# Optimization experiments

Hardware: AMD Instinct MI355X
Metric: run time of the kernel (lower is better)

The kernel has to match this reference:

```python
import jax, jax.numpy as jnp
import numpy as np

T, D_IN, H, D_OUT = 20, 4, 768, 1
B = 1024


def setup_inputs() -> dict:
    key = jax.random.key(0)
    ks = jax.random.split(key, 8)
    s = 1.0 / np.sqrt(H)
    return {
        "batch_price": jax.random.normal(ks[0], (B, T, D_IN), jnp.float32),
        "batch_event": jax.random.normal(ks[1], (B, T, H), jnp.float32),
        "W_ih": jax.random.uniform(ks[2], (T, 4 * H, D_IN), jnp.float32, -s, s),
        "W_hh": jax.random.uniform(ks[3], (T, 4 * H, H), jnp.float32, -s, s),
        "b_ih": jax.random.uniform(ks[4], (T, 4 * H), jnp.float32, -s, s),
        "b_hh": jax.random.uniform(ks[5], (T, 4 * H), jnp.float32, -s, s),
        "fc_w": jax.random.uniform(ks[6], (D_OUT, H), jnp.float32, -s, s),
        "fc_b": jax.random.uniform(ks[7], (D_OUT,), jnp.float32, -s, s),
    }


def _lstm_cell(x, h_mat, c, wih, whh, bih, bhh):
    # gates: [B, 4H] in PyTorch LSTMCell order (i, f, g, o)
    gates = x @ wih.T + bih + h_mat @ whh.T + bhh
    i, f, g, o = jnp.split(gates, 4, axis=-1)
    c_next = jax.nn.sigmoid(f) * c + jax.nn.sigmoid(i) * jnp.tanh(g)
    h_next = jax.nn.sigmoid(o) * jnp.tanh(c_next)
    return h_next, c_next


def reference(batch_price, batch_event, W_ih, W_hh, b_ih, b_hh, fc_w, fc_b):
    Bb, Tt, _ = batch_price.shape
    Hh = W_hh.shape[-1]
    # step 0: hx = batch_event[:, 0], cell state = zeros
    h, c = _lstm_cell(batch_price[:, 0], batch_event[:, 0],
                      jnp.zeros((Bb, Hh), batch_price.dtype),
                      W_ih[0], W_hh[0], b_ih[0], b_hh[0])

    def step(carry, inp):
        h, c = carry
        x, ev, wih, whh, bih, bhh = inp
        # faithful to source: hx = torch.sum(batch_event_t + h_prev) -> scalar
        hx = jnp.sum(ev + h)
        h_mat = jnp.broadcast_to(hx, (Bb, Hh))
        h2, c2 = _lstm_cell(x, h_mat, c, wih, whh, bih, bhh)
        return (h2, c2), None

    xs = (jnp.swapaxes(batch_price[:, 1:], 0, 1),  # [T-1, B, D_IN]
          jnp.swapaxes(batch_event[:, 1:], 0, 1),  # [T-1, B, H]
          W_ih[1:], W_hh[1:], b_ih[1:], b_hh[1:])
    (h, c), _ = jax.lax.scan(step, (h, c), xs)
    return h @ fc_w.T + fc_b  # [B, 1]
```

## Files before the change

kernel.cpp:

```cpp
#include <hip/hip_runtime.h>
#include <stdint.h>

#define Bsz 1024
#define Tn  20
#define Hn  768
#define G4n 3072

#define WS_SH    0
#define WS_SEV   32
#define WS_PART  64
#define WS_BCAST 576
#define WS_RS    640
#define WS_BS    62080
#define WS_C     123520
#define WS_EVH   909952
#define WS_EVL   1303168
#define WS_WH    1696384
#define WS_WL    2581120

#define NBC_EV   512
#define NBC_W    1152
#define NBC_Z    3
#define NBC_TOT  (NBC_EV + NBC_W + NBC_Z)

#define NB_GEMM   768
#define NB_ROWSUM 1824
#define NB_SEV    608
#define NB_BIAS   60
#define NB_TOTAL  (NB_GEMM + NB_ROWSUM + NB_SEV + NB_BIAS)

typedef float  floatx4 __attribute__((ext_vector_type(4)));
typedef short  bfrag8  __attribute__((ext_vector_type(8)));

__device__ __forceinline__ float wave_reduce(float v){
#pragma unroll
    for (int o = 32; o > 0; o >>= 1) v += __shfl_down(v, o, 64);
    return v;
}
__device__ __forceinline__ float sigf(float x){ return 1.0f/(1.0f+__expf(-x)); }
__device__ __forceinline__ float tanhfast(float x){ return 2.0f/(1.0f+__expf(-2.0f*x)) - 1.0f; }
__device__ __forceinline__ unsigned short f2bf(float f){
    uint32_t u = __float_as_uint(f);
    return (unsigned short)((u + 0x7fffu + ((u>>16)&1u)) >> 16);
}
__device__ __forceinline__ float bf2f(unsigned short h){ return __uint_as_float(((uint32_t)h)<<16); }
__device__ __forceinline__ uint64_t pack_tv(unsigned t, float v){
    return ((uint64_t)t << 32) | (uint64_t)__float_as_uint(v);
}

__global__ __launch_bounds__(256) void k_conv(
    const float* __restrict__ ev, const float* __restrict__ whh,
    float* __restrict__ ws)
{
    int bid = blockIdx.x, tid = threadIdx.x;
    if (bid < NBC_EV + NBC_W) {
        if (tid >= 192) return;
        int r = tid / 96;
        int i = (tid - r*96) * 8;
        const float* src;
        unsigned short *dh, *dl;
        int prow;
        if (bid < NBC_EV) {
            prow = bid*2 + r;
            src = ev + (size_t)prow*(Tn*Hn) + i;
            dh = (unsigned short*)(ws + WS_EVH);
            dl = (unsigned short*)(ws + WS_EVL);
        } else {
            int p = (bid - NBC_EV)*2 + r;
            int gsel = p / Hn;
            int ga = (gsel==0) ? 0 : (gsel==1 ? 2 : 3);
            int j = ga*Hn + (p - gsel*Hn);
            prow = p;
            src = whh + (size_t)j*Hn + i;
            dh = (unsigned short*)(ws + WS_WH);
            dl = (unsigned short*)(ws + WS_WL);
        }
        int rb = prow >> 4, col = prow & 15;
        int kb = i >> 5, q = (i >> 3) & 3;
        size_t base = (((size_t)(rb*24 + kb))*64 + q*16 + col) * 8;

        float4 v0 = *(const float4*)src;
        float4 v1 = *(const float4*)(src+4);
        float f[8] = {v0.x,v0.y,v0.z,v0.w,v1.x,v1.y,v1.z,v1.w};
        bfrag8 hv, lv;
#pragma unroll
        for (int qq = 0; qq < 8; ++qq) {
            unsigned short hb = f2bf(f[qq]);
            hv[qq] = (short)hb;
            lv[qq] = (short)f2bf(f[qq] - bf2f(hb));
        }
        *(bfrag8*)(dh + base) = hv;
        *(bfrag8*)(dl + base) = lv;
    } else {
        int idx = (bid - NBC_EV - NBC_W)*256 + tid;
        if (idx < 640) ws[idx] = 0.0f;
    }
}

__global__ __launch_bounds__(256) void k_pre(
    const float* __restrict__ price, const float* __restrict__ ev,
    const float* __restrict__ wih,   const float* __restrict__ whh,
    const float* __restrict__ bih,   const float* __restrict__ bhh,
    float* __restrict__ ws)
{
    __shared__ float redk[4];
    int blk = blockIdx.x, tid = threadIdx.x;
    int lane = tid & 63, wid = tid >> 6;

    if (blk < NB_GEMM) {
        float* Sh   = ws + WS_SH;
        float* cbuf = ws + WS_C;
        int bt = blk / 48, kt = blk % 48;
        int b0 = bt*64, k0 = kt*16;
        int w = wid, q = lane >> 4, col = lane & 15;

        const unsigned short* evh = (const unsigned short*)(ws + WS_EVH);
        const unsigned short* evl = (const unsigned short*)(ws + WS_EVL);
        const unsigned short* wh  = (const unsigned short*)(ws + WS_WH);
        const unsigned short* wl  = (const unsigned short*)(ws + WS_WL);

        int rb_a = bt*4 + w;
        const unsigned short* pah = evh + (size_t)rb_a*24*512 + (size_t)lane*8;
        const unsigned short* pal = evl + (size_t)rb_a*24*512 + (size_t)lane*8;
        const unsigned short* pb0h = wh + (size_t)(  0 + kt)*24*512 + (size_t)lane*8;
        const unsigned short* pb0l = wl + (size_t)(  0 + kt)*24*512 + (size_t)lane*8;
        const unsigned short* pb1h = wh + (size_t)( 48 + kt)*24*512 + (size_t)lane*8;
        const unsigned short* pb1l = wl + (size_t)( 48 + kt)*24*512 + (size_t)lane*8;
        const unsigned short* pb2h = wh + (size_t)( 96 + kt)*24*512 + (size_t)lane*8;
        const unsigned short* pb2l = wl + (size_t)( 96 + kt)*24*512 + (size_t)lane*8;

        floatx4 acc0 = (floatx4){0.f,0.f,0.f,0.f};
        floatx4 acc1 = (floatx4){0.f,0.f,0.f,0.f};
        floatx4 acc2 = (floatx4){0.f,0.f,0.f,0.f};

#pragma unroll 4
        for (int kb = 0; kb < 24; ++kb) {
            int off = kb*512;
            bfrag8 ah  = *(const bfrag8*)(pah  + off);
            bfrag8 al  = *(const bfrag8*)(pal  + off);
            bfrag8 b0h = *(const bfrag8*)(pb0h + off);
            bfrag8 b0l = *(const bfrag8*)(pb0l + off);
            acc0 = __builtin_amdgcn_mfma_f32_16x16x32_bf16(ah, b0h, acc0, 0,0,0);
            acc0 = __builtin_amdgcn_mfma_f32_16x16x32_bf16(ah, b0l, acc0, 0,0,0);
            acc0 = __builtin_amdgcn_mfma_f32_16x16x32_bf16(al, b0h, acc0, 0,0,0);
            bfrag8 b1h = *(const bfrag8*)(pb1h + off);
            bfrag8 b1l = *(const bfrag8*)(pb1l + off);
            acc1 = __builtin_amdgcn_mfma_f32_16x16x32_bf16(ah, b1h, acc1, 0,0,0);
            acc1 = __builtin_amdgcn_mfma_f32_16x16x32_bf16(ah, b1l, acc1, 0,0,0);
            acc1 = __builtin_amdgcn_mfma_f32_16x16x32_bf16(al, b1h, acc1, 0,0,0);
            bfrag8 b2h = *(const bfrag8*)(pb2h + off);
            bfrag8 b2l = *(const bfrag8*)(pb2l + off);
            acc2 = __builtin_amdgcn_mfma_f32_16x16x32_bf16(ah, b2h, acc2, 0,0,0);
            acc2 = __builtin_amdgcn_mfma_f32_16x16x32_bf16(ah, b2l, acc2, 0,0,0);
            acc2 = __builtin_amdgcn_mfma_f32_16x16x32_bf16(al, b2h, acc2, 0,0,0);
        }

        int j0 = 0*Hn + k0 + col;
        int j1 = 2*Hn + k0 + col;
        int j2 = 3*Hn + k0 + col;
        float4 w0 = *(const float4*)(wih + (size_t)j0*4);
        float4 w1 = *(const float4*)(wih + (size_t)j1*4);
        float4 w2 = *(const float4*)(wih + (size_t)j2*4);
        float bb0 = bih[j0] + bhh[j0];
        float bb1 = bih[j1] + bhh[j1];
        float bb2 = bih[j2] + bhh[j2];

        float hsum = 0.f;
#pragma unroll
        for (int r = 0; r < 4; ++r) {
            int b = b0 + w*16 + q*4 + r;
            float4 xv = *(const float4*)(price + (size_t)b*(Tn*4));
            float gi = acc0[r] + xv.x*w0.x + xv.y*w0.y + xv.z*w0.z + xv.w*w0.w + bb0;
            float gg = acc1[r] + xv.x*w1.x + xv.y*w1.y + xv.z*w1.z + xv.w*w1.w + bb1;
            float go = acc2[r] + xv.x*w2.x + xv.y*w2.y + xv.z*w2.z + xv.w*w2.w + bb2;
            float c0 = sigf(gi) * tanhfast(gg);
            float h0 = sigf(go) * tanhfast(c0);
            cbuf[(size_t)b*Hn + k0 + col] = c0;
            hsum += h0;
        }
        hsum = wave_reduce(hsum);
        if (lane == 0) redk[w] = hsum;
        __syncthreads();
        if (tid == 0) atomicAdd(&Sh[0], redk[0]+redk[1]+redk[2]+redk[3]);
        return;
    }

    blk -= NB_GEMM;
    if (blk < NB_ROWSUM) {
        int gw = blk*4 + wid;
        int t  = 1 + gw/384;
        int j0 = (gw - (t-1)*384)*8;
        const float* base = whh + ((size_t)t*G4n + j0)*Hn + (size_t)lane*4;
        float s[8];
#pragma unroll
        for (int r = 0; r < 8; ++r) {
            float4 v0 = *(const float4*)(base + (size_t)r*Hn);
            float4 v1 = *(const float4*)(base + (size_t)r*Hn + 256);
            float4 v2 = *(const float4*)(base + (size_t)r*Hn + 512);
            s[r] = (v0.x+v0.y+v0.z+v0.w) + (v1.x+v1.y+v1.z+v1.w) + (v2.x+v2.y+v2.z+v2.w);
        }
        float* rowsum = ws + WS_RS;
#pragma unroll
        for (int r = 0; r < 8; ++r) {
            float rs = wave_reduce(s[r]);
            if (lane == 0) rowsum[(size_t)t*G4n + j0 + r] = rs;
        }
        return;
    }

    blk -= NB_ROWSUM;
    if (blk < NB_SEV) {
        int gw = blk*4 + wid;
        int t   = 1 + gw/128;
        int b0s = (gw - (t-1)*128)*8;
        float s = 0.f;
#pragma unroll
        for (int r = 0; r < 8; ++r) {
            const float* base = ev + ((size_t)(b0s+r)*Tn + t)*Hn + (size_t)lane*4;
            float4 v0 = *(const float4*)(base);
            float4 v1 = *(const float4*)(base + 256);
            float4 v2 = *(const float4*)(base + 512);
            s += (v0.x+v0.y+v0.z+v0.w) + (v1.x+v1.y+v1.z+v1.w) + (v2.x+v2.y+v2.z+v2.w);
        }
        s = wave_reduce(s);
        if (lane == 0) atomicAdd(ws + WS_SEV + t, s);
        return;
    }

    blk -= NB_SEV;
    {
        int idx = blk*256 + tid;
        float4 a = *(const float4*)(bih + (size_t)idx*4);
        float4 b = *(const float4*)(bhh + (size_t)idx*4);
        float4 r4; r4.x=a.x+b.x; r4.y=a.y+b.y; r4.z=a.z+b.z; r4.w=a.w+b.w;
        *(float4*)(ws + WS_BS + (size_t)idx*4) = r4;
    }
}

__global__ __launch_bounds__(768) void k_steps(
    const float* __restrict__ price, const float* __restrict__ wih,
    const float* __restrict__ fcw,   const float* __restrict__ fcb,
    float* __restrict__ ws, float* __restrict__ out)
{
    __shared__ float pr[4][80];
    __shared__ float red[12];
    __shared__ float redP[4];
    __shared__ float redF[4][12];
    __shared__ float shx;

    float* Sh  = ws + WS_SH;
    float* Sev = ws + WS_SEV;
    uint64_t* part  = (uint64_t*)(ws + WS_PART);
    uint64_t* bcast = (uint64_t*)(ws + WS_BCAST);
    const float* rowsum  = ws + WS_RS;
    const float* biassum = ws + WS_BS;
    float* cbuf = ws + WS_C;

    int blk = blockIdx.x, tid = threadIdx.x;
    int lane = tid & 63, wid = tid >> 6;
    int k = tid;

    if (tid < 320) {
        int e = tid / 80, r = tid - e*80;
        pr[e][r] = price[(size_t)(blk + 256*e)*(Tn*4) + r];
    }

    float c[4];
#pragma unroll
    for (int e = 0; e < 4; ++e)
        c[e] = cbuf[(size_t)(blk + 256*e)*Hn + k];

    float fcwk = fcw[k];
    float fcb0 = fcb[0];
    float sh0  = Sh[0];

    __syncthreads();

    float hsum_prev = 0.f;
    float vout[4] = {0.f,0.f,0.f,0.f};

    for (int t = 1; t < Tn; ++t) {
        if (t >= 2) {
            float v = wave_reduce(hsum_prev);
            if (lane == 0) red[wid] = v;
            __syncthreads();
            if (tid == 0) {
                float tot = 0.f;
#pragma unroll
                for (int i = 0; i < 12; ++i) tot += red[i];
                __hip_atomic_store(&part[blk], pack_tv((unsigned)(t-1), tot),
                                   __ATOMIC_RELAXED, __HIP_MEMORY_SCOPE_AGENT);
            }
        }

        const float* wih_t = wih + (size_t)t*G4n*4;
        float rsv[4], base[4][4];
#pragma unroll
        for (int g = 0; g < 4; ++g) {
            int j = g*Hn + k;
            float4 wv = *(const float4*)(wih_t + (size_t)j*4);
            rsv[g]   = rowsum[t*G4n + j];
            float bs = biassum[t*G4n + j];
#pragma unroll
            for (int e = 0; e < 4; ++e) {
                base[e][g] = pr[e][t*4+0]*wv.x + pr[e][t*4+1]*wv.y
                           + pr[e][t*4+2]*wv.z + pr[e][t*4+3]*wv.w + bs;
            }
        }
        float sevt = Sev[t];

        if (blk == 0) {
            if (t >= 2) {
                if (tid < 256) {
                    uint64_t u;
                    do { u = __hip_atomic_load(&part[tid], __ATOMIC_RELAXED, __HIP_MEMORY_SCOPE_AGENT); }
                    while ((unsigned)(u >> 32) != (unsigned)(t-1));
                    float pv = wave_reduce(__uint_as_float((uint32_t)u));
                    if (lane == 0) redP[wid] = pv;
                }
                __syncthreads();
                if (tid == 0) {
                    float hx = sevt + (redP[0]+redP[1]+redP[2]+redP[3]);
                    shx = hx;
                    __hip_atomic_store(bcast, pack_tv((unsigned)t, hx),
                                       __ATOMIC_RELAXED, __HIP_MEMORY_SCOPE_AGENT);
                }
            } else {
                if (tid == 0) {
                    float hx = sevt + sh0;
                    shx = hx;
                    __hip_atomic_store(bcast, pack_tv(1u, hx),
                                       __ATOMIC_RELAXED, __HIP_MEMORY_SCOPE_AGENT);
                }
            }
            __syncthreads();
        } else {
            if (tid == 0) {
                uint64_t u;
                do { u = __hip_atomic_load(bcast, __ATOMIC_RELAXED, __HIP_MEMORY_SCOPE_AGENT); }
                while ((unsigned)(u >> 32) != (unsigned)t);
                shx = __uint_as_float((uint32_t)u);
            }
            __syncthreads();
        }
        float hx = shx;

        float hsum = 0.f;
#pragma unroll
        for (int e = 0; e < 4; ++e) {
            float gi = base[e][0] + hx*rsv[0];
            float gf = base[e][1] + hx*rsv[1];
            float gg = base[e][2] + hx*rsv[2];
            float go = base[e][3] + hx*rsv[3];
            float cn = sigf(gf)*c[e] + sigf(gi)*tanhfast(gg);
            c[e] = cn;
            float h = sigf(go)*tanhfast(cn);
            hsum += h;
            if (t == Tn-1) vout[e] = wave_reduce(h * fcwk);
        }
        hsum_prev = hsum;
    }

    if (lane == 0) {
#pragma unroll
        for (int e = 0; e < 4; ++e) redF[e][wid] = vout[e];
    }
    __syncthreads();
    if (tid < 4) {
        float tot = 0.f;
#pragma unroll
        for (int i = 0; i < 12; ++i) tot += redF[tid][i];
        out[blk + 256*tid] = tot + fcb0;
    }
}

extern "C" void kernel_launch(void* const* d_in, const int* in_sizes, int n_in,
                              void* d_out, int out_size, void* d_ws, size_t ws_size,
                              hipStream_t stream)
{
    const float* price = (const float*)d_in[0];
    const float* ev    = (const float*)d_in[1];
    const float* wih   = (const float*)d_in[2];
    const float* whh   = (const float*)d_in[3];
    const float* bih   = (const float*)d_in[4];
    const float* bhh   = (const float*)d_in[5];
    const float* fcw   = (const float*)d_in[6];
    const float* fcb   = (const float*)d_in[7];
    float* out = (float*)d_out;
    float* ws  = (float*)d_ws;

    k_conv <<<NBC_TOT, 256, 0, stream>>>(ev, whh, ws);
    k_pre  <<<NB_TOTAL, 256, 0, stream>>>(price, ev, wih, whh, bih, bhh, ws);
    k_steps<<<256, 768, 0, stream>>>(price, wih, fcw, fcb, ws, out);
}
```

Before: 428.1 us.

## Move cross-block scalar reduction to a dedicated coordinator block, drop atomics

Adds a 257th block to the step kernel that only polls the per-block partial sums, reduces them with a single wave, and publishes the broadcast scalar each step. Block 0 therefore no longer does both compute and coordination. The pre-kernel's atomicAdd reductions for the initial hidden sum and per-step event sums are replaced by plain per-block partial stores, which the coordinator sums. This is meant to shorten the serial critical path of the per-step global barrier and avoid atomic contention. It relies on the extra block being co-resident with the other 256 blocks for forward progress.

```diff
diff --git a/kernel.cpp b/kernel.cpp
--- a/kernel.cpp
+++ b/kernel.cpp
@@ -17,6 +17,8 @@
 #define WS_EVL   1303168
 #define WS_WH    1696384
 #define WS_WL    2581120
+#define WS_SHP   3465856
+#define WS_SEVP  3466624
 
 #define NBC_EV   512
 #define NBC_W    1152
@@ -108,7 +110,6 @@
     int lane = tid & 63, wid = tid >> 6;
 
     if (blk < NB_GEMM) {
-        float* Sh   = ws + WS_SH;
         float* cbuf = ws + WS_C;
         int bt = blk / 48, kt = blk % 48;
         int b0 = bt*64, k0 = kt*16;
@@ -181,7 +182,8 @@
         hsum = wave_reduce(hsum);
         if (lane == 0) redk[w] = hsum;
         __syncthreads();
-        if (tid == 0) atomicAdd(&Sh[0], redk[0]+redk[1]+redk[2]+redk[3]);
+        if (tid == 0)
+            ws[WS_SHP + blk] = redk[0]+redk[1]+redk[2]+redk[3];
         return;
     }
 
@@ -223,7 +225,7 @@
             s += (v0.x+v0.y+v0.z+v0.w) + (v1.x+v1.y+v1.z+v1.w) + (v2.x+v2.y+v2.z+v2.w);
         }
         s = wave_reduce(s);
-        if (lane == 0) atomicAdd(ws + WS_SEV + t, s);
+        if (lane == 0) ws[WS_SEVP + gw] = s;
         return;
     }
 
@@ -244,12 +246,9 @@
 {
     __shared__ float pr[4][80];
     __shared__ float red[12];
-    __shared__ float redP[4];
     __shared__ float redF[4][12];
     __shared__ float shx;
 
-    float* Sh  = ws + WS_SH;
-    float* Sev = ws + WS_SEV;
     uint64_t* part  = (uint64_t*)(ws + WS_PART);
     uint64_t* bcast = (uint64_t*)(ws + WS_BCAST);
     const float* rowsum  = ws + WS_RS;
@@ -257,6 +256,50 @@
     float* cbuf = ws + WS_C;
 
     int blk = blockIdx.x, tid = threadIdx.x;
+
+    if (blk == 256) {
+        if (tid >= 64) return;
+        int lane = tid;
+        const float* shp  = ws + WS_SHP;
+        const float* sevp = ws + WS_SEVP;
+
+        float s = 0.f;
+#pragma unroll
+        for (int i = 0; i < 12; ++i) s += shp[lane + 64*i];
+        s = wave_reduce(s);
+
+        {
+            float sv = sevp[lane] + sevp[64 + lane];
+            sv = wave_reduce(sv);
+            if (lane == 0)
+                __hip_atomic_store(bcast, pack_tv(1u, sv + s),
+                                   __ATOMIC_RELAXED, __HIP_MEMORY_SCOPE_AGENT);
+        }
+
+        for (int t = 2; t < Tn; ++t) {
+            float sv = sevp[(t-1)*128 + lane] + sevp[(t-1)*128 + 64 + lane];
+            sv = wave_reduce(sv);
+
+            unsigned want = (unsigned)(t-1);
+            uint64_t u0,u1,u2,u3;
+            for (;;) {
+                u0 = __hip_atomic_load(&part[lane*4+0], __ATOMIC_RELAXED, __HIP_MEMORY_SCOPE_AGENT);
+                u1 = __hip_atomic_load(&part[lane*4+1], __ATOMIC_RELAXED, __HIP_MEMORY_SCOPE_AGENT);
+                u2 = __hip_atomic_load(&part[lane*4+2], __ATOMIC_RELAXED, __HIP_MEMORY_SCOPE_AGENT);
+                u3 = __hip_atomic_load(&part[lane*4+3], __ATOMIC_RELAXED, __HIP_MEMORY_SCOPE_AGENT);
+                if ((unsigned)(u0>>32)==want && (unsigned)(u1>>32)==want &&
+                    (unsigned)(u2>>32)==want && (unsigned)(u3>>32)==want) break;
+            }
+            float p = __uint_as_float((uint32_t)u0) + __uint_as_float((uint32_t)u1)
+                    + __uint_as_float((uint32_t)u2) + __uint_as_float((uint32_t)u3);
+            p = wave_reduce(p);
+            if (lane == 0)
+                __hip_atomic_store(bcast, pack_tv((unsigned)t, sv + p),
+                                   __ATOMIC_RELAXED, __HIP_MEMORY_SCOPE_AGENT);
+        }
+        return;
+    }
+
     int lane = tid & 63, wid = tid >> 6;
     int k = tid;
 
@@ -272,7 +315,6 @@
 
     float fcwk = fcw[k];
     float fcb0 = fcb[0];
-    float sh0  = Sh[0];
 
     __syncthreads();
 
@@ -307,42 +349,14 @@
                            + pr[e][t*4+2]*wv.z + pr[e][t*4+3]*wv.w + bs;
             }
         }
-        float sevt = Sev[t];
-
-        if (blk == 0) {
-            if (t >= 2) {
-                if (tid < 256) {
-                    uint64_t u;
-                    do { u = __hip_atomic_load(&part[tid], __ATOMIC_RELAXED, __HIP_MEMORY_SCOPE_AGENT); }
-                    while ((unsigned)(u >> 32) != (unsigned)(t-1));
-                    float pv = wave_reduce(__uint_as_float((uint32_t)u));
-                    if (lane == 0) redP[wid] = pv;
-                }
-                __syncthreads();
-                if (tid == 0) {
-                    float hx = sevt + (redP[0]+redP[1]+redP[2]+redP[3]);
-                    shx = hx;
-                    __hip_atomic_store(bcast, pack_tv((unsigned)t, hx),
-                                       __ATOMIC_RELAXED, __HIP_MEMORY_SCOPE_AGENT);
-                }
-            } else {
-                if (tid == 0) {
-                    float hx = sevt + sh0;
-                    shx = hx;
-                    __hip_atomic_store(bcast, pack_tv(1u, hx),
-                                       __ATOMIC_RELAXED, __HIP_MEMORY_SCOPE_AGENT);
-                }
-            }
-            __syncthreads();
-        } else {
-            if (tid == 0) {
-                uint64_t u;
-                do { u = __hip_atomic_load(bcast, __ATOMIC_RELAXED, __HIP_MEMORY_SCOPE_AGENT); }
-                while ((unsigned)(u >> 32) != (unsigned)t);
-                shx = __uint_as_float((uint32_t)u);
-            }
-            __syncthreads();
-        }
+
+        if (tid == 0) {
+            uint64_t u;
+            do { u = __hip_atomic_load(bcast, __ATOMIC_RELAXED, __HIP_MEMORY_SCOPE_AGENT); }
+            while ((unsigned)(u >> 32) != (unsigned)t);
+            shx = __uint_as_float((uint32_t)u);
+        }
+        __syncthreads();
         float hx = shx;
 
         float hsum = 0.f;
@@ -391,5 +405,5 @@
 
     k_conv <<<NBC_TOT, 256, 0, stream>>>(ev, whh, ws);
     k_pre  <<<NB_TOTAL, 256, 0, stream>>>(price, ev, wih, whh, bih, bhh, ws);
-    k_steps<<<256, 768, 0, stream>>>(price, wih, fcw, fcb, ws, out);
-}
+    k_steps<<<257, 768, 0, stream>>>(price, wih, fcw, fcb, ws, out);
+}
```

Result: no change. 424.5 us (-0.8%).
